# Optimization experiments

Hardware: AMD Instinct MI355X
Metric: run time of the kernel (lower is better)

## Reference

```python
import jax, jax.numpy as jnp
import numpy as np
import math

B, S, D, H = 2, 2048, 2048, 16
HD = D // H  # head_dim = 128
NEG = -9e15


def setup_inputs() -> dict:
    key = jax.random.key(0)
    k1, k2, k3 = jax.random.split(key, 3)
    x = jax.random.normal(k1, (B, S, D), dtype=jnp.float32)
    Wqkv = jax.random.normal(k2, (D, 3 * D), dtype=jnp.float32) * (1.0 / math.sqrt(D))
    bqkv = jnp.zeros((3 * D,), dtype=jnp.float32)
    Wo = jax.random.normal(k3, (D, D), dtype=jnp.float32) * (1.0 / math.sqrt(D))
    bo = jnp.zeros((D,), dtype=jnp.float32)
    return {"x": x, "Wqkv": Wqkv, "bqkv": bqkv, "Wo": Wo, "bo": bo}


def reference(x, Wqkv, bqkv, Wo, bo):
    b, s, d = x.shape
    # fused QKV projection
    qkv = x @ Wqkv + bqkv                       # [B,S,3D]
    qkv = qkv.reshape(b, s, H, 3 * HD)          # per-head interleaved q|k|v
    qkv = qkv.transpose(0, 2, 1, 3)             # [B,H,S,3*HD]
    q, k, v = jnp.split(qkv, 3, axis=-1)        # each [B,H,S,HD]
    scale = 1.0 / math.sqrt(HD)
    logits = jnp.einsum('bhqd,bhkd->bhqk', q, k) * scale  # [B,H,S,S]
    causal = jnp.tril(jnp.ones((s, s), dtype=bool))[None, None]
    logits = jnp.where(causal, logits, NEG)
    score = jax.nn.softmax(logits, axis=-1)
    attn = jnp.einsum('bhqk,bhkd->bhqd', score, v)         # [B,H,S,HD]
    attn = attn.transpose(0, 2, 1, 3).reshape(b, s, d)
    return attn @ Wo + bo
```

## Files before the change

kernel.cpp:

```cpp
#include <hip/hip_runtime.h>
#include <stdint.h>

#define DEV static __device__ __forceinline__

typedef _Float16 half8 __attribute__((ext_vector_type(8)));
typedef _Float16 half4 __attribute__((ext_vector_type(4)));
typedef float f32x4 __attribute__((ext_vector_type(4)));
typedef uint16_t u16x8 __attribute__((ext_vector_type(8)));

constexpr int Bc = 2, Sc = 2048, Dc = 2048, Hc = 16, HDc = 128;
constexpr int D3c = 3 * Dc;
constexpr int Mc = Bc * Sc;

DEV void gl_lds16(const void* g, void* l) {
    __builtin_amdgcn_global_load_lds(
        (const __attribute__((address_space(1))) unsigned int*)g,
        (__attribute__((address_space(3))) unsigned int*)l,
        16, 0, 0);
}

DEV void transpose_tile(const float* __restrict__ in, _Float16* __restrict__ out,
                        int R, int C, int bx, int by, int t)
{
    __shared__ float ls[64][64];
    const int r0 = by * 64, c0 = bx * 64;
    {
        const int rr = t >> 4, lc = t & 15;
#pragma unroll
        for (int p = 0; p < 4; ++p) {
            int r = p * 16 + rr;
            int pc = lc ^ ((r >> 3) & 7);
            *(float4*)&ls[r][pc * 4] =
                *(const float4*)&in[(size_t)(r0 + r) * C + c0 + lc * 4];
        }
    }
    __syncthreads();
    {
        const int oc = t >> 3, ss = (t & 7) * 8;
#pragma unroll
        for (int p = 0; p < 2; ++p) {
            int c = p * 32 + oc;
            int lc = c >> 2, wi = c & 3;
            half8 hv;
#pragma unroll
            for (int j = 0; j < 8; ++j) {
                int r = ss + j;
                hv[j] = (_Float16)ls[r][(lc ^ ((r >> 3) & 7)) * 4 + wi];
            }
            *(half8*)&out[(size_t)(c0 + c) * R + r0 + ss] = hv;
        }
    }
}

__global__ __launch_bounds__(256) void prep_kernel(
    const float* __restrict__ x, const float* __restrict__ Wqkv,
    const float* __restrict__ Wo,
    _Float16* __restrict__ xb, _Float16* __restrict__ wt1,
    _Float16* __restrict__ wt2)
{
    const int id = blockIdx.x, t = threadIdx.x;
    if (id < 4096) {
        int i = id * 256 + t;
        const float4* p = (const float4*)x;
        float4 a = p[i * 2], b = p[i * 2 + 1];
        half8 hv;
        hv[0] = (_Float16)a.x; hv[1] = (_Float16)a.y; hv[2] = (_Float16)a.z; hv[3] = (_Float16)a.w;
        hv[4] = (_Float16)b.x; hv[5] = (_Float16)b.y; hv[6] = (_Float16)b.z; hv[7] = (_Float16)b.w;
        *(half8*)(xb + (size_t)i * 8) = hv;
    } else if (id < 4096 + 3072) {
        int id2 = id - 4096;
        transpose_tile(Wqkv, wt1, Dc, D3c, id2 % 96, id2 / 96, t);
    } else {
        int id3 = id - 7168;
        transpose_tile(Wo, wt2, Dc, Dc, id3 & 31, id3 >> 5, t);
    }
}

__global__ __launch_bounds__(256) void transpose_v_kernel(
    const uint16_t* __restrict__ qkv, uint16_t* __restrict__ vt)
{
    __shared__ uint16_t ls[64][64];
    const int t = threadIdx.x;
    const int s0 = blockIdx.x * 64, d0 = blockIdx.y * 64, bh = blockIdx.z;
    const int b = bh >> 4, h = bh & 15;
    {
        const int sr = t >> 3, lc = t & 7;
#pragma unroll
        for (int p = 0; p < 2; ++p) {
            int s = p * 32 + sr;
            int pc = lc ^ ((s >> 3) & 7);
            *(u16x8*)&ls[s][pc * 8] =
                *(const u16x8*)&qkv[(size_t)(b * Sc + s0 + s) * D3c + h * 384 + 256 + d0 + lc * 8];
        }
    }
    __syncthreads();
    {
        const int od = t >> 3, ss = (t & 7) * 8;
#pragma unroll
        for (int p = 0; p < 2; ++p) {
            int d = p * 32 + od;
            int lc = d >> 3, wi = d & 7;
            u16x8 hv;
#pragma unroll
            for (int j = 0; j < 8; ++j) {
                int s = ss + j;
                hv[j] = ls[s][(lc ^ ((s >> 3) & 7)) * 8 + wi];
            }
            *(u16x8*)&vt[(size_t)(bh * HDc + d0 + d) * Sc + s0 + ss] = hv;
        }
    }
}

template <int BF16OUT>
__global__ __launch_bounds__(256, 2) void gemm_bt_kernel(
    const _Float16* __restrict__ A, const _Float16* __restrict__ Bt,
    const float* __restrict__ bias, void* __restrict__ Cout,
    int M, int N, int K)
{
    __shared__ __align__(16) char smem[32768];
    char* sA = smem;
    char* sB = smem + 16384;
    const int t = threadIdx.x, w = t >> 6, lane = t & 63;
    const int quad = lane >> 4, l15 = lane & 15;
    const int wr = w >> 1, wc = w & 1;
    const int n0 = blockIdx.x * 128, m0 = blockIdx.y * 128;

    const f32x4 vzero = {0.f, 0.f, 0.f, 0.f};
    f32x4 acc[4][4];
#pragma unroll
    for (int i = 0; i < 4; ++i)
#pragma unroll
        for (int j = 0; j < 4; ++j) acc[i][j] = vzero;

    const int kiters = K >> 6;
    for (int kk = 0; kk < kiters; ++kk) {
#pragma unroll
        for (int i = 0; i < 4; ++i) {
            int c = i * 256 + t;
            int row = c >> 3, kbs = c & 7, kact = kbs ^ (row & 7);
            gl_lds16(A + (size_t)(m0 + row) * K + kk * 64 + kact * 8,
                     sA + (i * 256 + w * 64) * 16);
        }
#pragma unroll
        for (int i = 0; i < 4; ++i) {
            int c = i * 256 + t;
            int row = c >> 3, kbs = c & 7, kact = kbs ^ (row & 7);
            gl_lds16(Bt + (size_t)(n0 + row) * K + kk * 64 + kact * 8,
                     sB + (i * 256 + w * 64) * 16);
        }
        __syncthreads();
#pragma unroll
        for (int ks = 0; ks < 2; ++ks) {
            half8 af[4], bf[4];
#pragma unroll
            for (int mt = 0; mt < 4; ++mt) {
                int row = wr * 64 + mt * 16 + l15;
                int kact = (ks * 4 + quad) ^ (l15 & 7);
                af[mt] = *(const half8*)(sA + row * 128 + kact * 16);
            }
#pragma unroll
            for (int nt = 0; nt < 4; ++nt) {
                int row = wc * 64 + nt * 16 + l15;
                int kact = (ks * 4 + quad) ^ (l15 & 7);
                bf[nt] = *(const half8*)(sB + row * 128 + kact * 16);
            }
#pragma unroll
            for (int mt = 0; mt < 4; ++mt)
#pragma unroll
                for (int nt = 0; nt < 4; ++nt)
                    acc[mt][nt] = __builtin_amdgcn_mfma_f32_16x16x32_f16(
                        af[mt], bf[nt], acc[mt][nt], 0, 0, 0);
        }
        __syncthreads();
    }

#pragma unroll
    for (int nt = 0; nt < 4; ++nt) {
        int col = n0 + wc * 64 + nt * 16 + l15;
        float bv = bias[col];
#pragma unroll
        for (int mt = 0; mt < 4; ++mt)
#pragma unroll
            for (int r = 0; r < 4; ++r) {
                int row = m0 + wr * 64 + mt * 16 + quad * 4 + r;
                float v = acc[mt][nt][r] + bv;
                if (BF16OUT) ((_Float16*)Cout)[(size_t)row * N + col] = (_Float16)v;
                else         ((float*)Cout)[(size_t)row * N + col] = v;
            }
    }
}

__global__ __launch_bounds__(512, 4) void flash_kernel(
    const _Float16* __restrict__ qkv, const _Float16* __restrict__ vt,
    _Float16* __restrict__ attn)
{
    __shared__ __align__(16) char smem[36864];
    char* sK = smem;
    char* sV = smem + 16384;

    const int t = threadIdx.x, w = t >> 6, lane = t & 63;
    const int quad = lane >> 4, l15 = lane & 15;
    const int bh = blockIdx.x;
    const int by = blockIdx.y;
    const int qt = (by < 8) ? 15 - by : by - 8;
    const int b = bh >> 4, h = bh & 15;
    const int q0 = qt * 128;
    const int qrow = q0 + w * 16 + l15;

    half8 qf[4];
#pragma unroll
    for (int ks = 0; ks < 4; ++ks) {
        const _Float16* p = qkv + (size_t)(b * Sc + qrow) * D3c +
                            h * 384 + ks * 32 + quad * 8;
        qf[ks] = *(const half8*)p;
    }

    const f32x4 vzero = {0.f, 0.f, 0.f, 0.f};
    f32x4 o[8];
#pragma unroll
    for (int dt = 0; dt < 8; ++dt) o[dt] = vzero;
    float m_st = -1e30f, l_st = 0.f;

    const float kScale = 0.08838834764831845f * 1.4426950408889634f;
    const int nkt = 2 * qt + 2;

    for (int kt = 0; kt < nkt; ++kt) {
#pragma unroll
        for (int i = 0; i < 2; ++i) {
            int c = i * 512 + t;
            int row = c >> 4, kbs = c & 15, kact = kbs ^ (row & 15);
            gl_lds16(qkv + (size_t)(b * Sc + kt * 64 + row) * D3c + h * 384 + 128 + kact * 8,
                     sK + (i * 512 + w * 64) * 16);
        }
#pragma unroll
        for (int i = 0; i < 2; ++i) {
            int c = i * 512 + t;
            int row = c >> 3, kbs = c & 7, kact = kbs ^ (row & 7);
            gl_lds16(vt + (size_t)(bh * HDc + row) * Sc + kt * 64 + kact * 8,
                     sV + (i * 512 + w * 64) * 16);
        }
        __syncthreads();

        f32x4 sf[4];
#pragma unroll
        for (int kb = 0; kb < 4; ++kb) sf[kb] = vzero;
#pragma unroll
        for (int ks = 0; ks < 4; ++ks) {
#pragma unroll
            for (int kb = 0; kb < 4; ++kb) {
                int row = kb * 16 + l15;
                int slot = (ks * 4 + quad) ^ l15;
                half8 kf = *(const half8*)(sK + row * 256 + slot * 16);
                sf[kb] = __builtin_amdgcn_mfma_f32_16x16x32_f16(kf, qf[ks], sf[kb], 0, 0, 0);
            }
        }

        const bool domask = (kt >= 2 * qt);
        float rm = -1e30f;
#pragma unroll
        for (int kb = 0; kb < 4; ++kb)
#pragma unroll
            for (int r = 0; r < 4; ++r) {
                float v = sf[kb][r] * kScale;
                if (domask) {
                    int col = kt * 64 + kb * 16 + quad * 4 + r;
                    if (col > qrow) v = -1e30f;
                }
                sf[kb][r] = v;
                rm = fmaxf(rm, v);
            }
        rm = fmaxf(rm, __shfl_xor(rm, 16, 64));
        rm = fmaxf(rm, __shfl_xor(rm, 32, 64));
        float mn = fmaxf(m_st, rm);
        float alpha = __builtin_amdgcn_exp2f(m_st - mn);
        m_st = mn;

        half4 pb[4];
        float rs = 0.f;
#pragma unroll
        for (int kb = 0; kb < 4; ++kb)
#pragma unroll
            for (int r = 0; r < 4; ++r) {
                float p = __builtin_amdgcn_exp2f(sf[kb][r] - mn);
                rs += p;
                pb[kb][r] = (_Float16)p;
            }
        rs += __shfl_xor(rs, 16, 64);
        rs += __shfl_xor(rs, 32, 64);
        l_st = l_st * alpha + rs;

#pragma unroll
        for (int dt = 0; dt < 8; ++dt)
#pragma unroll
            for (int r = 0; r < 4; ++r) o[dt][r] *= alpha;

#pragma unroll
        for (int kb = 0; kb < 4; ++kb) {
#pragma unroll
            for (int dt = 0; dt < 8; ++dt) {
                int row = dt * 16 + l15;
                int slot = (kb * 2 + (quad >> 1)) ^ (l15 & 7);
                half4 vf = *(const half4*)(sV + row * 128 + slot * 16 + (quad & 1) * 8);
                o[dt] = __builtin_amdgcn_mfma_f32_16x16x16f16(vf, pb[kb], o[dt], 0, 0, 0);
            }
        }
        __syncthreads();
    }

    char* sO = smem;
    float linv = 1.0f / l_st;
#pragma unroll
    for (int dt = 0; dt < 8; ++dt) {
        half4 hv;
#pragma unroll
        for (int r = 0; r < 4; ++r) hv[r] = (_Float16)(o[dt][r] * linv);
        *(half4*)(sO + (w * 16 + l15) * 272 + (dt * 16 + quad * 4) * 2) = hv;
    }
    __syncthreads();
#pragma unroll
    for (int i = 0; i < 4; ++i) {
        int q = i * 32 + (t >> 4);
        int d = (t & 15) * 8;
        half8 hv = *(const half8*)(sO + q * 272 + d * 2);
        *(half8*)(attn + (size_t)(b * Sc + q0 + q) * Dc + h * HDc + d) = hv;
    }
}

extern "C" void kernel_launch(void* const* d_in, const int* in_sizes, int n_in,
                              void* d_out, int out_size, void* d_ws, size_t ws_size,
                              hipStream_t stream)
{
    (void)in_sizes; (void)n_in; (void)out_size; (void)ws_size;
    const float* x    = (const float*)d_in[0];
    const float* Wqkv = (const float*)d_in[1];
    const float* bqkv = (const float*)d_in[2];
    const float* Wo   = (const float*)d_in[3];
    const float* bo   = (const float*)d_in[4];
    float* out = (float*)d_out;

    _Float16* xb  = (_Float16*)d_ws;
    _Float16* wt1 = xb  + (size_t)Mc * Dc;
    _Float16* wt2 = wt1 + (size_t)D3c * Dc;
    _Float16* qkv = wt2 + (size_t)Dc * Dc;
    _Float16* vtg  = wt1;
    _Float16* attn = xb;

    prep_kernel<<<8192, 256, 0, stream>>>(x, Wqkv, Wo, xb, wt1, wt2);
    gemm_bt_kernel<1><<<dim3(D3c / 128, Mc / 128), 256, 0, stream>>>(
        xb, wt1, bqkv, qkv, Mc, D3c, Dc);
    transpose_v_kernel<<<dim3(Sc / 64, 2, Bc * Hc), 256, 0, stream>>>(
        (const uint16_t*)qkv, (uint16_t*)vtg);
    flash_kernel<<<dim3(Bc * Hc, 16), 512, 0, stream>>>(qkv, vtg, attn);
    gemm_bt_kernel<0><<<dim3(Dc / 128, Mc / 128), 256, 0, stream>>>(
        attn, wt2, bo, out, Mc, Dc, Dc);
}
```

Before: 360.4 us.

## Fuse V transpose into QKV GEMM epilogue, drop transpose kernel

The QKV GEMM epilogue now writes V tiles already transposed (d-major over sequence) into the V slot of the qkv buffer, and the flash kernel reads V from that relocated layout. This removes the separate transpose_v kernel launch and its extra read/write pass over V. In exchange the V epilogue uses scattered half4 stores with a strided address map, and the flash kernel's V loads compute more complex addresses.

```diff
diff --git a/kernel.cpp b/kernel.cpp
--- a/kernel.cpp
+++ b/kernel.cpp
@@ -11,6 +11,7 @@
 constexpr int Bc = 2, Sc = 2048, Dc = 2048, Hc = 16, HDc = 128;
 constexpr int D3c = 3 * Dc;
 constexpr int Mc = Bc * Sc;
+
 
 DEV void gl_lds16(const void* g, void* l) {
     __builtin_amdgcn_global_load_lds(
@@ -76,41 +77,6 @@
     }
 }
 
-__global__ __launch_bounds__(256) void transpose_v_kernel(
-    const uint16_t* __restrict__ qkv, uint16_t* __restrict__ vt)
-{
-    __shared__ uint16_t ls[64][64];
-    const int t = threadIdx.x;
-    const int s0 = blockIdx.x * 64, d0 = blockIdx.y * 64, bh = blockIdx.z;
-    const int b = bh >> 4, h = bh & 15;
-    {
-        const int sr = t >> 3, lc = t & 7;
-#pragma unroll
-        for (int p = 0; p < 2; ++p) {
-            int s = p * 32 + sr;
-            int pc = lc ^ ((s >> 3) & 7);
-            *(u16x8*)&ls[s][pc * 8] =
-                *(const u16x8*)&qkv[(size_t)(b * Sc + s0 + s) * D3c + h * 384 + 256 + d0 + lc * 8];
-        }
-    }
-    __syncthreads();
-    {
-        const int od = t >> 3, ss = (t & 7) * 8;
-#pragma unroll
-        for (int p = 0; p < 2; ++p) {
-            int d = p * 32 + od;
-            int lc = d >> 3, wi = d & 7;
-            u16x8 hv;
-#pragma unroll
-            for (int j = 0; j < 8; ++j) {
-                int s = ss + j;
-                hv[j] = ls[s][(lc ^ ((s >> 3) & 7)) * 8 + wi];
-            }
-            *(u16x8*)&vt[(size_t)(bh * HDc + d0 + d) * Sc + s0 + ss] = hv;
-        }
-    }
-}
-
 template <int BF16OUT>
 __global__ __launch_bounds__(256, 2) void gemm_bt_kernel(
     const _Float16* __restrict__ A, const _Float16* __restrict__ Bt,
@@ -174,25 +140,47 @@
         __syncthreads();
     }
 
-#pragma unroll
-    for (int nt = 0; nt < 4; ++nt) {
-        int col = n0 + wc * 64 + nt * 16 + l15;
-        float bv = bias[col];
-#pragma unroll
-        for (int mt = 0; mt < 4; ++mt)
-#pragma unroll
-            for (int r = 0; r < 4; ++r) {
-                int row = m0 + wr * 64 + mt * 16 + quad * 4 + r;
-                float v = acc[mt][nt][r] + bv;
-                if (BF16OUT) ((_Float16*)Cout)[(size_t)row * N + col] = (_Float16)v;
-                else         ((float*)Cout)[(size_t)row * N + col] = v;
-            }
+    const bool isV = BF16OUT && ((n0 % 384) == 256);
+    if (isV) {
+        const int hh = n0 / 384;
+        _Float16* vb = (_Float16*)Cout;
+#pragma unroll
+        for (int nt = 0; nt < 4; ++nt) {
+            int d = wc * 64 + nt * 16 + l15;
+            float bv = bias[n0 + d];
+#pragma unroll
+            for (int mt = 0; mt < 4; ++mt) {
+                int rowb = m0 + wr * 64 + mt * 16 + quad * 4;
+                int bb = rowb >> 11, sg = rowb & 2047;
+                int q = d * 256 + (sg >> 3);
+                half4 hv;
+#pragma unroll
+                for (int r = 0; r < 4; ++r) hv[r] = (_Float16)(acc[mt][nt][r] + bv);
+                _Float16* dst = vb + (size_t)(bb * Sc + (q >> 4)) * D3c +
+                                hh * 384 + 256 + (q & 15) * 8 + (sg & 7);
+                *(half4*)dst = hv;
+            }
+        }
+    } else {
+#pragma unroll
+        for (int nt = 0; nt < 4; ++nt) {
+            int col = n0 + wc * 64 + nt * 16 + l15;
+            float bv = bias[col];
+#pragma unroll
+            for (int mt = 0; mt < 4; ++mt)
+#pragma unroll
+                for (int r = 0; r < 4; ++r) {
+                    int row = m0 + wr * 64 + mt * 16 + quad * 4 + r;
+                    float v = acc[mt][nt][r] + bv;
+                    if (BF16OUT) ((_Float16*)Cout)[(size_t)row * N + col] = (_Float16)v;
+                    else         ((float*)Cout)[(size_t)row * N + col] = v;
+                }
+        }
     }
 }
 
 __global__ __launch_bounds__(512, 4) void flash_kernel(
-    const _Float16* __restrict__ qkv, const _Float16* __restrict__ vt,
-    _Float16* __restrict__ attn)
+    const _Float16* __restrict__ qkv, _Float16* __restrict__ attn)
 {
     __shared__ __align__(16) char smem[36864];
     char* sK = smem;
@@ -236,7 +224,8 @@
         for (int i = 0; i < 2; ++i) {
             int c = i * 512 + t;
             int row = c >> 3, kbs = c & 7, kact = kbs ^ (row & 7);
-            gl_lds16(vt + (size_t)(bh * HDc + row) * Sc + kt * 64 + kact * 8,
+            int q = row * 256 + kt * 8 + kact;
+            gl_lds16(qkv + (size_t)(b * Sc + (q >> 4)) * D3c + h * 384 + 256 + (q & 15) * 8,
                      sV + (i * 512 + w * 64) * 16);
         }
         __syncthreads();
@@ -342,15 +331,12 @@
     _Float16* wt1 = xb  + (size_t)Mc * Dc;
     _Float16* wt2 = wt1 + (size_t)D3c * Dc;
     _Float16* qkv = wt2 + (size_t)Dc * Dc;
-    _Float16* vtg  = wt1;
     _Float16* attn = xb;
 
     prep_kernel<<<8192, 256, 0, stream>>>(x, Wqkv, Wo, xb, wt1, wt2);
     gemm_bt_kernel<1><<<dim3(D3c / 128, Mc / 128), 256, 0, stream>>>(
         xb, wt1, bqkv, qkv, Mc, D3c, Dc);
-    transpose_v_kernel<<<dim3(Sc / 64, 2, Bc * Hc), 256, 0, stream>>>(
-        (const uint16_t*)qkv, (uint16_t*)vtg);
-    flash_kernel<<<dim3(Bc * Hc, 16), 512, 0, stream>>>(qkv, vtg, attn);
+    flash_kernel<<<dim3(Bc * Hc, 16), 512, 0, stream>>>(qkv, attn);
     gemm_bt_kernel<0><<<dim3(Dc / 128, Mc / 128), 256, 0, stream>>>(
         attn, wt2, bo, out, Mc, Dc, Dc);
 }
```

Result: no change. 357.6 us (-0.8%).
